# Optimization experiments

Hardware: AMD Instinct MI355X
Metric: run time of the kernel (lower is better)

Reference implementation:

```python
import jax, jax.numpy as jnp
import numpy as np

PI = np.pi

def dct_2_1d(x):
    # DCT-II over last dim, norm=None, matching the torch FFT-based impl.
    N = x.shape[-1]
    v = jnp.concatenate([x[..., ::2], jnp.flip(x[..., 1::2], axis=-1)], axis=-1)
    Vc = jnp.fft.fft(v, axis=-1)
    k = -jnp.arange(N, dtype=x.dtype) * PI / (2 * N)
    V = Vc.real * jnp.cos(k) - Vc.imag * jnp.sin(k)
    return 2 * V

def idct_2_1d(X):
    # Inverse of dct_2_1d (scaled DCT-III), norm=None.
    N = X.shape[-1]
    X_v = X / 2
    k = jnp.arange(N, dtype=X.dtype) * PI / (2 * N)
    W_r, W_i = jnp.cos(k), jnp.sin(k)
    V_t_r = X_v
    V_t_i = jnp.concatenate([jnp.zeros_like(X_v[..., :1]), -jnp.flip(X_v, axis=-1)[..., :-1]], axis=-1)
    V_r = V_t_r * W_r - V_t_i * W_i
    V_i = V_t_r * W_i + V_t_i * W_r
    # torch.fft.irfft(complex, n=N) uses the first N//2+1 entries; numpy/jax irfft crops the same way.
    v = jnp.fft.irfft(V_r + 1j * V_i, n=N, axis=-1)
    x = jnp.zeros_like(v)
    x = x.at[..., ::2].set(v[..., :N - N // 2])
    x = x.at[..., 1::2].set(jnp.flip(v, axis=-1)[..., :N // 2])
    return x

def setup_inputs() -> dict:
    key = jax.random.key(0)
    k1, k2 = jax.random.split(key)
    B, N, C = 256, 196, 768  # N = h*w = 14*14, C = dim
    x = jax.random.normal(k1, (B, N, C), dtype=jnp.float32)
    weight = jax.random.normal(k2, (C, N), dtype=jnp.float32) * 0.02
    return {"x": x, "weight": weight}

def reference(x, weight):
    # x: [B, N, C]; weight: [C, N]
    xt = jnp.transpose(x, (0, 2, 1)).astype(jnp.float32)  # [B, C, N]
    X = dct_2_1d(xt)
    X = X * weight  # broadcast [C, N] over batch
    y = idct_2_1d(X)
    return jnp.transpose(y, (0, 2, 1))  # [B, N, C]
```

## Files before the change

kernel.cpp:

```cpp
#include <hip/hip_runtime.h>

typedef __bf16 bf16;
typedef __bf16 bf16x8 __attribute__((ext_vector_type(8)));
typedef __bf16 bf16x4 __attribute__((ext_vector_type(4)));
typedef float f32x4 __attribute__((ext_vector_type(4)));

#define N_DIM 196
#define C_DIM 768
#define B_DIM 256
#define KSTEPS 7
#define MT1 14
#define MT2 13
#define CT 64
#define LPITCH 232

#define D2F_ELEMS (MT1 * KSTEPS * 512)
#define EF_ELEMS  (MT2 * KSTEPS * 512)

__global__ void init_mats(bf16* __restrict__ d2f, bf16* __restrict__ ef) {
    int idx = blockIdx.x * 256 + threadIdx.x;
    const float PI = 3.14159265358979323846f;
    if (idx < D2F_ELEMS) {
        int j    = idx & 7;
        int lane = (idx >> 3) & 63;
        int rest = idx >> 9;
        int ks = rest % KSTEPS;
        int mt = rest / KSTEPS;
        int row = mt * 16 + (lane & 15);
        int col = ks * 32 + (lane >> 4) * 8 + j;
        float v = 0.0f;
        if (row < N_DIM && col < N_DIM) {
            int t = ((2 * col + 1) * row) % (4 * N_DIM);
            v = 2.0f * cosf(PI * (float)t / (float)(2 * N_DIM));
        }
        d2f[idx] = (bf16)v;
    } else {
        int e = idx - D2F_ELEMS;
        if (e < EF_ELEMS) {
            int j    = e & 7;
            int lane = (e >> 3) & 63;
            int rest = e >> 9;
            int ks = rest % KSTEPS;
            int mt = rest / KSTEPS;
            int row = mt * 16 + (lane & 15);
            int col = ks * 32 + (lane >> 4) * 8 + j;
            float v = 0.0f;
            if (row < N_DIM && col < N_DIM) {
                if (col == 0) {
                    v = 1.0f / (float)(2 * N_DIM);
                } else {
                    int t = ((2 * row + 1) * col) % (4 * N_DIM);
                    v = cosf(PI * (float)t / (float)(2 * N_DIM)) / (float)N_DIM;
                }
            }
            ef[e] = (bf16)v;
        }
    }
}

__global__ __launch_bounds__(256) void dct_fused(
        const float* __restrict__ x, const float* __restrict__ wgt,
        const bf16* __restrict__ d2f, const bf16* __restrict__ ef,
        float* __restrict__ out) {
    __shared__ bf16 lds[CT * LPITCH];

    const int b  = blockIdx.y;
    const int c0 = blockIdx.x * CT;
    const int t  = threadIdx.x;
    const int wave = t >> 6;
    const int lane = t & 63;
    const int ln15 = lane & 15;
    const int q    = lane >> 4;

    {
        int cj   = (t & 15) * 4;
        int mrow = t >> 4;
        for (int i = 0; i < MT1; ++i) {
            int m = i * 16 + mrow;
            float4 v = make_float4(0.f, 0.f, 0.f, 0.f);
            if (m < N_DIM)
                v = *(const float4*)(x + ((size_t)b * N_DIM + m) * C_DIM + c0 + cj);
            lds[(cj + 0) * LPITCH + m] = (bf16)v.x;
            lds[(cj + 1) * LPITCH + m] = (bf16)v.y;
            lds[(cj + 2) * LPITCH + m] = (bf16)v.z;
            lds[(cj + 3) * LPITCH + m] = (bf16)v.w;
        }
    }
    __syncthreads();

    f32x4 acc[4][4] = {};
    for (int ks = 0; ks < KSTEPS; ++ks) {
        bf16x8 bfr[4];
#pragma unroll
        for (int ct = 0; ct < 4; ++ct)
            bfr[ct] = *(const bf16x8*)(lds + (ct * 16 + ln15) * LPITCH + ks * 32 + q * 8);
#pragma unroll
        for (int ml = 0; ml < 4; ++ml) {
            int mt = wave + 4 * ml;
            if (mt < MT1) {
                bf16x8 afr = *(const bf16x8*)(d2f + ((size_t)(mt * KSTEPS + ks) * 64 + lane) * 8);
#pragma unroll
                for (int ct = 0; ct < 4; ++ct)
                    acc[ml][ct] = __builtin_amdgcn_mfma_f32_16x16x32_bf16(afr, bfr[ct], acc[ml][ct], 0, 0, 0);
            }
        }
    }
    __syncthreads();

#pragma unroll
    for (int ml = 0; ml < 4; ++ml) {
        int mt = wave + 4 * ml;
        if (mt >= MT1) continue;
        int kb = mt * 16 + q * 4;
#pragma unroll
        for (int ct = 0; ct < 4; ++ct) {
            int cc = ct * 16 + ln15;
            float4 wv = make_float4(0.f, 0.f, 0.f, 0.f);
            if (kb < N_DIM)
                wv = *(const float4*)(wgt + (size_t)(c0 + cc) * N_DIM + kb);
            bf16x4 pv;
            pv[0] = (bf16)(acc[ml][ct][0] * wv.x);
            pv[1] = (bf16)(acc[ml][ct][1] * wv.y);
            pv[2] = (bf16)(acc[ml][ct][2] * wv.z);
            pv[3] = (bf16)(acc[ml][ct][3] * wv.w);
            *(bf16x4*)(lds + cc * LPITCH + kb) = pv;
        }
    }
    __syncthreads();

    f32x4 acc2[4][4] = {};
    for (int ks = 0; ks < KSTEPS; ++ks) {
        bf16x8 bfr[4];
#pragma unroll
        for (int ct = 0; ct < 4; ++ct)
            bfr[ct] = *(const bf16x8*)(lds + (ct * 16 + ln15) * LPITCH + ks * 32 + q * 8);
#pragma unroll
        for (int ml = 0; ml < 4; ++ml) {
            int mt = wave + 4 * ml;
            if (mt < MT2) {
                bf16x8 afr = *(const bf16x8*)(ef + ((size_t)(mt * KSTEPS + ks) * 64 + lane) * 8);
#pragma unroll
                for (int ct = 0; ct < 4; ++ct)
                    acc2[ml][ct] = __builtin_amdgcn_mfma_f32_16x16x32_bf16(afr, bfr[ct], acc2[ml][ct], 0, 0, 0);
            }
        }
    }

#pragma unroll
    for (int ml = 0; ml < 4; ++ml) {
        int mt = wave + 4 * ml;
        if (mt >= MT2) continue;
#pragma unroll
        for (int ct = 0; ct < 4; ++ct) {
            int cc = ct * 16 + ln15;
#pragma unroll
            for (int r = 0; r < 4; ++r) {
                int n = mt * 16 + q * 4 + r;
                if (n < N_DIM)
                    out[((size_t)b * N_DIM + n) * C_DIM + c0 + cc] = acc2[ml][ct][r];
            }
        }
    }
}

extern "C" void kernel_launch(void* const* d_in, const int* in_sizes, int n_in,
                              void* d_out, int out_size, void* d_ws, size_t ws_size,
                              hipStream_t stream) {
    const float* x   = (const float*)d_in[0];
    const float* wgt = (const float*)d_in[1];
    float* out = (float*)d_out;

    bf16* d2f = (bf16*)d_ws;
    bf16* ef  = d2f + D2F_ELEMS;

    int tot = D2F_ELEMS + EF_ELEMS;
    init_mats<<<(tot + 255) / 256, 256, 0, stream>>>(d2f, ef);

    dim3 grid(C_DIM / CT, B_DIM);
    dct_fused<<<grid, 256, 0, stream>>>(x, wgt, d2f, ef, out);
}
```

Baseline: 343.1 us.

## Use transposing LDS reads for x tile and swap GEMM2 operands for vector stores

The x staging now writes 8-wide bf16 vectors into an m-major swizzled LDS layout instead of scattered 2-byte transposing stores. The first GEMM reads B fragments with ds_read_b64_tr_b16, which transposes them in hardware. The second GEMM swaps the A and B operands so each lane's accumulator holds four consecutive channels, which allows float4 output stores instead of scalar ones. It also adds an explicit waitcnt and a sched_barrier. Together these target LDS bank conflicts and uncoalesced global stores, but they rely on inline asm for a gfx950-specific instruction.

```diff
diff --git a/kernel.cpp b/kernel.cpp
--- a/kernel.cpp
+++ b/kernel.cpp
@@ -1,4 +1,5 @@
 #include <hip/hip_runtime.h>
+#include <stdint.h>
 
 typedef __bf16 bf16;
 typedef __bf16 bf16x8 __attribute__((ext_vector_type(8)));
@@ -58,6 +59,9 @@
     }
 }
 
+#define TRRD(dst, a, imm) \
+    asm volatile("ds_read_b64_tr_b16 %0, %1 offset:" #imm : "=v"(dst) : "v"(a))
+
 __global__ __launch_bounds__(256) void dct_fused(
         const float* __restrict__ x, const float* __restrict__ wgt,
         const bf16* __restrict__ d2f, const bf16* __restrict__ ef,
@@ -73,35 +77,60 @@
     const int q    = lane >> 4;
 
     {
-        int cj   = (t & 15) * 4;
-        int mrow = t >> 4;
-        for (int i = 0; i < MT1; ++i) {
-            int m = i * 16 + mrow;
-            float4 v = make_float4(0.f, 0.f, 0.f, 0.f);
-            if (m < N_DIM)
-                v = *(const float4*)(x + ((size_t)b * N_DIM + m) * C_DIM + c0 + cj);
-            lds[(cj + 0) * LPITCH + m] = (bf16)v.x;
-            lds[(cj + 1) * LPITCH + m] = (bf16)v.y;
-            lds[(cj + 2) * LPITCH + m] = (bf16)v.z;
-            lds[(cj + 3) * LPITCH + m] = (bf16)v.w;
+        const int cg8 = t & 7;
+        const int mr  = t >> 3;
+        const float* xp = x + (size_t)b * N_DIM * C_DIM + c0 + cg8 * 8;
+#pragma unroll
+        for (int i = 0; i < KSTEPS; ++i) {
+            int m = i * 32 + mr;
+            float4 v0 = make_float4(0.f, 0.f, 0.f, 0.f);
+            float4 v1 = v0;
+            if (m < N_DIM) {
+                v0 = *(const float4*)(xp + (size_t)m * C_DIM);
+                v1 = *(const float4*)(xp + (size_t)m * C_DIM + 4);
+            }
+            bf16x8 pv;
+            pv[0] = (bf16)v0.x; pv[1] = (bf16)v0.y; pv[2] = (bf16)v0.z; pv[3] = (bf16)v0.w;
+            pv[4] = (bf16)v1.x; pv[5] = (bf16)v1.y; pv[6] = (bf16)v1.z; pv[7] = (bf16)v1.w;
+            *(bf16x8*)(lds + ((m >> 2) * 4 + (cg8 >> 1)) * 64 + (m & 3) * 16 + (cg8 & 1) * 8) = pv;
         }
     }
     __syncthreads();
 
     f32x4 acc[4][4] = {};
-    for (int ks = 0; ks < KSTEPS; ++ks) {
-        bf16x8 bfr[4];
-#pragma unroll
-        for (int ct = 0; ct < 4; ++ct)
-            bfr[ct] = *(const bf16x8*)(lds + (ct * 16 + ln15) * LPITCH + ks * 32 + q * 8);
-#pragma unroll
-        for (int ml = 0; ml < 4; ++ml) {
-            int mt = wave + 4 * ml;
-            if (mt < MT1) {
-                bf16x8 afr = *(const bf16x8*)(d2f + ((size_t)(mt * KSTEPS + ks) * 64 + lane) * 8);
-#pragma unroll
-                for (int ct = 0; ct < 4; ++ct)
-                    acc[ml][ct] = __builtin_amdgcn_mfma_f32_16x16x32_bf16(afr, bfr[ct], acc[ml][ct], 0, 0, 0);
+    {
+        const uint32_t xaddr = (uint32_t)(size_t)&lds[0] + q * 1024 + ln15 * 8;
+#pragma unroll
+        for (int ks = 0; ks < KSTEPS; ++ks) {
+            uint32_t a = xaddr + ks * 4096;
+            bf16x4 l0, l1, l2, l3, h0, h1, h2, h3;
+            TRRD(l0, a, 0);   TRRD(h0, a, 512);
+            TRRD(l1, a, 128); TRRD(h1, a, 640);
+            TRRD(l2, a, 256); TRRD(h2, a, 768);
+            TRRD(l3, a, 384); TRRD(h3, a, 896);
+            bf16x8 afr[4];
+#pragma unroll
+            for (int ml = 0; ml < 4; ++ml) {
+                int mt = wave + 4 * ml;
+                if (mt < MT1)
+                    afr[ml] = *(const bf16x8*)(d2f + ((size_t)(mt * KSTEPS + ks) * 64 + lane) * 8);
+            }
+            asm volatile("s_waitcnt lgkmcnt(0)");
+            __builtin_amdgcn_sched_barrier(0);
+            bf16x8 bb[4];
+            bb[0] = __builtin_shufflevector(l0, h0, 0, 1, 2, 3, 4, 5, 6, 7);
+            bb[1] = __builtin_shufflevector(l1, h1, 0, 1, 2, 3, 4, 5, 6, 7);
+            bb[2] = __builtin_shufflevector(l2, h2, 0, 1, 2, 3, 4, 5, 6, 7);
+            bb[3] = __builtin_shufflevector(l3, h3, 0, 1, 2, 3, 4, 5, 6, 7);
+#pragma unroll
+            for (int ml = 0; ml < 4; ++ml) {
+                int mt = wave + 4 * ml;
+                if (mt < MT1) {
+#pragma unroll
+                    for (int ct = 0; ct < 4; ++ct)
+                        acc[ml][ct] = __builtin_amdgcn_mfma_f32_16x16x32_bf16(
+                            afr[ml], bb[ct], acc[ml][ct], 0, 0, 0);
+                }
             }
         }
     }
@@ -129,36 +158,35 @@
     __syncthreads();
 
     f32x4 acc2[4][4] = {};
+#pragma unroll
     for (int ks = 0; ks < KSTEPS; ++ks) {
-        bf16x8 bfr[4];
+        bf16x8 afr2[4];
 #pragma unroll
         for (int ct = 0; ct < 4; ++ct)
-            bfr[ct] = *(const bf16x8*)(lds + (ct * 16 + ln15) * LPITCH + ks * 32 + q * 8);
-#pragma unroll
-        for (int ml = 0; ml < 4; ++ml) {
-            int mt = wave + 4 * ml;
-            if (mt < MT2) {
-                bf16x8 afr = *(const bf16x8*)(ef + ((size_t)(mt * KSTEPS + ks) * 64 + lane) * 8);
+            afr2[ct] = *(const bf16x8*)(lds + (ct * 16 + ln15) * LPITCH + ks * 32 + q * 8);
+#pragma unroll
+        for (int i = 0; i < 4; ++i) {
+            int nt = wave + 4 * i;
+            if (nt < MT2) {
+                bf16x8 bfr = *(const bf16x8*)(ef + ((size_t)(nt * KSTEPS + ks) * 64 + lane) * 8);
 #pragma unroll
                 for (int ct = 0; ct < 4; ++ct)
-                    acc2[ml][ct] = __builtin_amdgcn_mfma_f32_16x16x32_bf16(afr, bfr[ct], acc2[ml][ct], 0, 0, 0);
-            }
-        }
-    }
-
-#pragma unroll
-    for (int ml = 0; ml < 4; ++ml) {
-        int mt = wave + 4 * ml;
-        if (mt >= MT2) continue;
-#pragma unroll
-        for (int ct = 0; ct < 4; ++ct) {
-            int cc = ct * 16 + ln15;
-#pragma unroll
-            for (int r = 0; r < 4; ++r) {
-                int n = mt * 16 + q * 4 + r;
-                if (n < N_DIM)
-                    out[((size_t)b * N_DIM + n) * C_DIM + c0 + cc] = acc2[ml][ct][r];
-            }
+                    acc2[i][ct] = __builtin_amdgcn_mfma_f32_16x16x32_bf16(
+                        afr2[ct], bfr, acc2[i][ct], 0, 0, 0);
+            }
+        }
+    }
+
+#pragma unroll
+    for (int i = 0; i < 4; ++i) {
+        int nt = wave + 4 * i;
+        if (nt >= MT2) continue;
+        int n = nt * 16 + ln15;
+        if (n < N_DIM) {
+#pragma unroll
+            for (int ct = 0; ct < 4; ++ct)
+                *(f32x4*)(out + ((size_t)b * N_DIM + n) * C_DIM + c0 + ct * 16 + q * 4) =
+                    acc2[i][ct];
         }
     }
 }
```

After: 326.3 us. 4.9% less time.
